# Kernel tuning notes

Measured on AMD Instinct MI355X. Metric: run time of the kernel, lower is better.

## Reference

```python
import jax, jax.numpy as jnp
import numpy as np

B, T, H, DQK, DV = 2, 8192, 8, 128, 128
HID = H * DQK  # 1024
CHUNK = 64
EPS = 1e-5


def hedgehog(x, w, b):
    # torch Linear: y = x @ W.T + b, then softmax over cat([2y, -2y])
    y = x @ w.T + b
    return jax.nn.softmax(jnp.concatenate([2.0 * y, -2.0 * y], axis=-1), axis=-1)


def rmsnorm(x):
    return x * jax.lax.rsqrt(jnp.mean(x * x, axis=-1, keepdims=True) + EPS)


def chunk_linear_attn(q, k, v):
    # q, k: [B, T, H, Dk]; v: [B, T, H, Dv]  (head_first=False)
    scale = q.shape[-1] ** -0.5
    q = q * scale
    Bq, Tq, Hq, Dk = q.shape
    Dv = v.shape[-1]
    nc = Tq // CHUNK

    def to_chunks(t):
        # [B, T, H, D] -> [nc, B, H, C, D]
        return t.reshape(Bq, nc, CHUNK, Hq, -1).transpose(1, 0, 3, 2, 4)

    qc, kc, vc = to_chunks(q), to_chunks(k), to_chunks(v)
    mask = jnp.tril(jnp.ones((CHUNK, CHUNK), dtype=bool))

    def step(S, qkv):
        qi, ki, vi = qkv  # [B, H, C, D]
        attn = jnp.einsum('bhcd,bhed->bhce', qi, ki)      # intra-chunk scores
        attn = jnp.where(mask, attn, 0.0)                 # causal within chunk
        o = jnp.einsum('bhce,bhev->bhcv', attn, vi) \
            + jnp.einsum('bhcd,bhdv->bhcv', qi, S)        # inter-chunk via state
        S = S + jnp.einsum('bhcd,bhcv->bhdv', ki, vi)
        return S, o

    S0 = jnp.zeros((Bq, Hq, Dk, Dv), q.dtype)
    _, oc = jax.lax.scan(step, S0, (qc, kc, vc))          # oc: [nc, B, H, C, Dv]
    return oc.transpose(1, 0, 3, 2, 4).reshape(Bq, Tq, Hq, Dv)


def setup_inputs() -> dict:
    key = jax.random.key(0)
    ks = jax.random.split(key, 9)
    gain = 2.0 ** (-2.5)

    def xavier(k, shape):
        bound = gain * np.sqrt(6.0 / (shape[0] + shape[1]))
        return jax.random.uniform(k, shape, jnp.float32, -bound, bound)

    return {
        'x': jax.random.normal(ks[0], (B, T, HID), jnp.float32),
        'Wq': xavier(ks[1], (HID, HID)),
        'Wk': xavier(ks[2], (HID, HID)),
        'Wv': xavier(ks[3], (HID, HID)),
        'Wo': xavier(ks[4], (HID, HID)),
        # self.apply xavier-inits the hedgehog Linear layers too (no _is_hf_initialized flag)
        'fmq_w': xavier(ks[5], (DQK, DQK)),
        'fmq_b': jnp.zeros((DQK,), jnp.float32),
        'fmk_w': xavier(ks[6], (DQK, DQK)),
        'fmk_b': jnp.zeros((DQK,), jnp.float32),
    }


def reference(x, Wq, Wk, Wv, Wo, fmq_w, fmq_b, fmk_w, fmk_b):
    q = (x @ Wq.T).reshape(B, T, H, DQK)
    k = (x @ Wk.T).reshape(B, T, H, DQK)
    v = (x @ Wv.T).reshape(B, T, H, DV)
    q = hedgehog(q, fmq_w, fmq_b)   # [B, T, H, 2*DQK]
    k = hedgehog(k, fmk_w, fmk_b)   # [B, T, H, 2*DQK]
    o = chunk_linear_attn(q, k, v)  # [B, T, H, DV]
    o = rmsnorm(o.reshape(B, T, H * DV))
    return o @ Wo.T
```

## Files before the change

kernel.cpp:

```cpp
#include <hip/hip_runtime.h>
#include <stdint.h>

typedef unsigned short u16;
typedef __bf16 bf16x8 __attribute__((ext_vector_type(8)));
typedef float f32x4 __attribute__((ext_vector_type(4)));
typedef float f32x16 __attribute__((ext_vector_type(16)));

__device__ __forceinline__ u16 f2b(float f) {
  union { float f; unsigned u; } v; v.f = f;
  unsigned r = v.u + 0x7fffu + ((v.u >> 16) & 1u);
  return (u16)(r >> 16);
}
__device__ __forceinline__ float b2f(u16 b) {
  union { unsigned u; float f; } v; v.u = ((unsigned)b) << 16;
  return v.f;
}

__global__ __launch_bounds__(256) void cast_bf16(const float* __restrict__ in,
                                                 u16* __restrict__ out, int n4) {
  int i = blockIdx.x * 256 + threadIdx.x;
  if (i >= n4) return;
  float4 f = ((const float4*)in)[i];
  ushort4 r = make_ushort4(f2b(f.x), f2b(f.y), f2b(f.z), f2b(f.w));
  ((ushort4*)out)[i] = r;
}

__global__ __launch_bounds__(256) void fold_w(const float* __restrict__ W,
                                              const float* __restrict__ fmw,
                                              u16* __restrict__ out) {
  int hj = blockIdx.x;
  int h = hj >> 7, j = hj & 127;
  int i0 = threadIdx.x * 4;
  float a0 = 0.f, a1 = 0.f, a2 = 0.f, a3 = 0.f;
  const float* Wh = W + (size_t)(h * 128) * 1024 + i0;
  const float* fw = fmw + j * 128;
  for (int d = 0; d < 128; ++d) {
    float wv = fw[d];
    const float* wr = Wh + (size_t)d * 1024;
    a0 += wv * wr[0]; a1 += wv * wr[1]; a2 += wv * wr[2]; a3 += wv * wr[3];
  }
  ushort4 r = make_ushort4(f2b(a0), f2b(a1), f2b(a2), f2b(a3));
  ((ushort4*)(out + (size_t)hj * 1024))[threadIdx.x] = r;
}

template <int OUT_BF16>
__global__ __launch_bounds__(256) void gemm_bt(const u16* __restrict__ A,
                                               const u16* __restrict__ B,
                                               void* __restrict__ Cv,
                                               int M, int N, int K, int SWZ, int LNT) {
  __shared__ u16 smem[16384];
  u16* As = smem;
  u16* Bs = smem + 8192;
  const int tid = threadIdx.x;
  int g = blockIdx.y * gridDim.x + blockIdx.x;
  int xcd = g & 7, local = g >> 3;
  int mt, nt;
  if (SWZ == 0) {
    mt = xcd * ((int)gridDim.y >> 3) + (local >> LNT);
    nt = local & ((1 << LNT) - 1);
  } else {
    nt = xcd * ((int)gridDim.x >> 3) + (local >> 3);
    mt = local & 7;
  }
  const int m0 = mt * 128, n0 = nt * 128;
  const int wave = tid >> 6, lane = tid & 63;
  const int wm = (wave >> 1) << 6, wn = (wave & 1) << 6;
  f32x4 acc[4][4] = {};
  const int srow = tid >> 3;
  const int scol = (tid & 7) << 3;
  const u16* Ab = A + (size_t)(m0 + srow) * K + scol;
  const u16* Bb = B + (size_t)(n0 + srow) * K + scol;
  u16* Asp = As + srow * 64 + scol;
  u16* Bsp = Bs + srow * 64 + scol;
  const int fm = lane & 15;
  const int fk = (lane >> 4) << 3;
  for (int kt = 0; kt < K; kt += 64) {
#pragma unroll
    for (int i = 0; i < 4; ++i) {
      __builtin_amdgcn_global_load_lds(
          (__attribute__((address_space(1))) unsigned int*)(Ab + (size_t)i * 32 * K + kt),
          (__attribute__((address_space(3))) unsigned int*)(Asp + i * 32 * 64), 16, 0, 0);
      __builtin_amdgcn_global_load_lds(
          (__attribute__((address_space(1))) unsigned int*)(Bb + (size_t)i * 32 * K + kt),
          (__attribute__((address_space(3))) unsigned int*)(Bsp + i * 32 * 64), 16, 0, 0);
    }
    __syncthreads();
#pragma unroll
    for (int kb = 0; kb < 2; ++kb) {
      bf16x8 af[4], bfr[4];
#pragma unroll
      for (int i = 0; i < 4; ++i)
        af[i] = *(const bf16x8*)(As + (wm + i * 16 + fm) * 64 + kb * 32 + fk);
#pragma unroll
      for (int j = 0; j < 4; ++j)
        bfr[j] = *(const bf16x8*)(Bs + (wn + j * 16 + fm) * 64 + kb * 32 + fk);
#pragma unroll
      for (int i = 0; i < 4; ++i)
#pragma unroll
        for (int j = 0; j < 4; ++j)
          acc[i][j] = __builtin_amdgcn_mfma_f32_16x16x32_bf16(af[i], bfr[j], acc[i][j], 0, 0, 0);
    }
    __syncthreads();
  }
  const int cr = (lane >> 4) << 2;
  const int cc = lane & 15;
  if (OUT_BF16) {
    u16* Cs = smem;
#pragma unroll
    for (int i = 0; i < 4; ++i)
#pragma unroll
      for (int j = 0; j < 4; ++j)
#pragma unroll
        for (int r = 0; r < 4; ++r)
          Cs[(wm + i * 16 + cr + r) * 128 + wn + j * 16 + cc] = f2b(acc[i][j][r]);
    __syncthreads();
    u16* Cg = (u16*)Cv;
#pragma unroll
    for (int i = 0; i < 8; ++i) {
      int row = (i >> 1) * 32 + (tid >> 3);
      int col = ((i & 1) * 8 + (tid & 7)) * 8;
      *(uint4*)(Cg + (size_t)(m0 + row) * N + n0 + col) = *(const uint4*)(Cs + row * 128 + col);
    }
  } else {
    float* Csf = (float*)smem;
    float* Cg = (float*)Cv;
#pragma unroll
    for (int hh = 0; hh < 2; ++hh) {
      __syncthreads();
      if ((wm >> 6) == hh) {
#pragma unroll
        for (int i = 0; i < 4; ++i)
#pragma unroll
          for (int j = 0; j < 4; ++j)
#pragma unroll
            for (int r = 0; r < 4; ++r)
              Csf[(i * 16 + cr + r) * 128 + wn + j * 16 + cc] = acc[i][j][r];
      }
      __syncthreads();
#pragma unroll
      for (int i = 0; i < 8; ++i) {
        int row = (i >> 1) * 16 + (tid >> 4);
        int col = ((i & 1) * 16 + (tid & 15)) * 4;
        *(float4*)(Cg + (size_t)(m0 + hh * 64 + row) * N + n0 + col) =
            *(const float4*)(Csf + row * 128 + col);
      }
    }
  }
}

__global__ __launch_bounds__(256) void hedgehog_sm(const u16* __restrict__ y,
                                                   const float* __restrict__ bias,
                                                   u16* __restrict__ phi, float scale,
                                                   int colbase) {
  int wave = threadIdx.x >> 6, lane = threadIdx.x & 63;
  int rh = blockIdx.x * 4 + wave;
  const u16* yr = y + (size_t)(rh >> 3) * 2048 + colbase + (rh & 7) * 128;
  float a1 = 2.f * (b2f(yr[lane]) + bias[lane]);
  float a2 = 2.f * (b2f(yr[lane + 64]) + bias[lane + 64]);
  float mx = fmaxf(fabsf(a1), fabsf(a2));
#pragma unroll
  for (int off = 32; off; off >>= 1) mx = fmaxf(mx, __shfl_xor(mx, off, 64));
  float e1 = __expf(a1 - mx), e2 = __expf(a2 - mx);
  float n1 = __expf(-a1 - mx), n2 = __expf(-a2 - mx);
  float s = e1 + e2 + n1 + n2;
#pragma unroll
  for (int off = 32; off; off >>= 1) s += __shfl_xor(s, off, 64);
  float inv = scale / s;
  u16* pr = phi + (size_t)rh * 256;
  pr[lane] = f2b(e1 * inv);
  pr[lane + 64] = f2b(e2 * inv);
  pr[lane + 128] = f2b(n1 * inv);
  pr[lane + 192] = f2b(n2 * inv);
}

__global__ __launch_bounds__(256, 1) void attn_intra_kv2(const u16* __restrict__ phi_q,
                                                         const u16* __restrict__ phi_k,
                                                         const u16* __restrict__ vt,
                                                         float* __restrict__ o,
                                                         u16* __restrict__ kv) {
  __shared__ u16 lds[18432];
  u16* At = lds;
  u16* Kt = lds;
  int g = blockIdx.x;
  int n = g & 63, h = g >> 6;
  int t0 = n * 128;
  const u16* qg = phi_q + ((size_t)t0 * 8 + h) * 256;
  const u16* kg = phi_k + ((size_t)t0 * 8 + h) * 256;
  const u16* vg = vt + (size_t)(h * 128) * 8192 + t0;
  int tid = threadIdx.x, lane = tid & 63, w = tid >> 6;
  const int fr = lane & 31, fg = (lane >> 5) << 3;
  const int rbase = (lane >> 5) << 2;
  const int mw = (w >> 1) << 6;
  const int nw = (w & 1) << 6;

  f32x16 accS[2][2] = {};
#pragma unroll
  for (int ks = 0; ks < 16; ++ks) {
    bf16x8 a[2], b[2];
#pragma unroll
    for (int i = 0; i < 2; ++i)
      a[i] = *(const bf16x8*)(qg + (size_t)(mw + i * 32 + fr) * 2048 + ks * 16 + fg);
#pragma unroll
    for (int j = 0; j < 2; ++j)
      b[j] = *(const bf16x8*)(kg + (size_t)(nw + j * 32 + fr) * 2048 + ks * 16 + fg);
#pragma unroll
    for (int i = 0; i < 2; ++i)
#pragma unroll
      for (int j = 0; j < 2; ++j)
        accS[i][j] = __builtin_amdgcn_mfma_f32_32x32x16_bf16(a[i], b[j], accS[i][j], 0, 0, 0);
  }
#pragma unroll
  for (int i = 0; i < 2; ++i)
#pragma unroll
    for (int j = 0; j < 2; ++j) {
      int col = nw + j * 32 + (lane & 31);
#pragma unroll
      for (int r = 0; r < 16; ++r) {
        int row = mw + i * 32 + (r & 3) + ((r >> 2) << 3) + rbase;
        At[row * 136 + col] = f2b(col <= row ? accS[i][j][r] : 0.f);
      }
    }
  __syncthreads();
  f32x16 accO[2][2] = {};
#pragma unroll
  for (int ks = 0; ks < 8; ++ks) {
    bf16x8 a[2], b[2];
#pragma unroll
    for (int i = 0; i < 2; ++i)
      a[i] = *(const bf16x8*)(At + (mw + i * 32 + fr) * 136 + ks * 16 + fg);
#pragma unroll
    for (int j = 0; j < 2; ++j)
      b[j] = *(const bf16x8*)(vg + (size_t)(nw + j * 32 + fr) * 8192 + ks * 16 + fg);
#pragma unroll
    for (int i = 0; i < 2; ++i)
#pragma unroll
      for (int j = 0; j < 2; ++j)
        accO[i][j] = __builtin_amdgcn_mfma_f32_32x32x16_bf16(a[i], b[j], accO[i][j], 0, 0, 0);
  }
  {
    float* og = o + ((size_t)t0 * 8 + h) * 128;
#pragma unroll
    for (int i = 0; i < 2; ++i)
#pragma unroll
      for (int j = 0; j < 2; ++j) {
        int vc = nw + j * 32 + (lane & 31);
#pragma unroll
        for (int r = 0; r < 16; ++r) {
          int row = mw + i * 32 + (r & 3) + ((r >> 2) << 3) + rbase;
          og[(size_t)row * 1024 + vc] = accO[i][j][r];
        }
      }
  }
  __syncthreads();

  const int nd = w << 6;
  f32x16 accKV[4][2] = {};
#pragma unroll
  for (int hb = 0; hb < 2; ++hb) {
    {
      int r4 = (tid & 15) << 2;
      int d0 = (tid >> 4) << 4;
      u16 tmp[4][16];
#pragma unroll
      for (int r = 0; r < 4; ++r) {
        const u16* src = kg + (size_t)(hb * 64 + r4 + r) * 2048 + d0;
        *(uint4*)(tmp[r]) = *(const uint4*)src;
        *(uint4*)(tmp[r] + 8) = *(const uint4*)(src + 8);
      }
#pragma unroll
      for (int jj = 0; jj < 16; ++jj) {
        ushort4 pk = make_ushort4(tmp[0][jj], tmp[1][jj], tmp[2][jj], tmp[3][jj]);
        *(ushort4*)(Kt + (d0 + jj) * 72 + r4) = pk;
      }
    }
    __syncthreads();
#pragma unroll
    for (int ks = 0; ks < 4; ++ks) {
      bf16x8 a[4], b[2];
#pragma unroll
      for (int mi = 0; mi < 4; ++mi)
        a[mi] = *(const bf16x8*)(vg + (size_t)(mi * 32 + fr) * 8192 + hb * 64 + ks * 16 + fg);
#pragma unroll
      for (int nj = 0; nj < 2; ++nj)
        b[nj] = *(const bf16x8*)(Kt + (nd + nj * 32 + fr) * 72 + ks * 16 + fg);
#pragma unroll
      for (int mi = 0; mi < 4; ++mi)
#pragma unroll
        for (int nj = 0; nj < 2; ++nj)
          accKV[mi][nj] =
              __builtin_amdgcn_mfma_f32_32x32x16_bf16(a[mi], b[nj], accKV[mi][nj], 0, 0, 0);
    }
    __syncthreads();
  }
  {
    u16* kvg = kv + (size_t)g * 32768;
#pragma unroll
    for (int mi = 0; mi < 4; ++mi)
#pragma unroll
      for (int nj = 0; nj < 2; ++nj) {
        f32x16 acc = accKV[mi][nj];
        int d = nd + nj * 32 + (lane & 31);
#pragma unroll
        for (int r = 0; r < 16; ++r) {
          int vc = mi * 32 + (r & 3) + ((r >> 2) << 3) + rbase;
          kvg[(size_t)vc * 256 + d] = f2b(acc[r]);
        }
      }
  }
}

__global__ __launch_bounds__(256) void kv_scan2(u16* __restrict__ kv) {
  int idx = blockIdx.x * 256 + threadIdx.x;
  int h = idx >> 13;
  int e4 = idx & 8191;
  u16* p = kv + (size_t)h * 2097152 + (size_t)e4 * 4;
  float run[4] = {};
  for (int nn = 0; nn < 64; ++nn) {
    uint2 raw = *(const uint2*)p;
    u16* rv = (u16*)&raw;
    uint2 outw;
    u16* ov = (u16*)&outw;
#pragma unroll
    for (int i = 0; i < 4; ++i) {
      float v = b2f(rv[i]);
      ov[i] = f2b(run[i]);
      run[i] += v;
    }
    *(uint2*)p = outw;
    p += 32768;
  }
}

__global__ __launch_bounds__(256, 1) void attn_inter2(const u16* __restrict__ phi_q,
                                                      const u16* __restrict__ kv,
                                                      float* __restrict__ o) {
  int g = blockIdx.x;
  int n = g & 63, h = g >> 6;
  int t0 = n * 128;
  const u16* qg = phi_q + ((size_t)t0 * 8 + h) * 256;
  const u16* sg = kv + (size_t)g * 32768;
  int tid = threadIdx.x, lane = tid & 63, w = tid >> 6;
  const int fr = lane & 31, fg = (lane >> 5) << 3;
  const int rbase = (lane >> 5) << 2;
  const int mw = (w >> 1) << 6;
  const int nw = (w & 1) << 6;
  f32x16 acc[2][2] = {};
#pragma unroll
  for (int ks = 0; ks < 16; ++ks) {
    bf16x8 a[2], b[2];
#pragma unroll
    for (int i = 0; i < 2; ++i)
      a[i] = *(const bf16x8*)(qg + (size_t)(mw + i * 32 + fr) * 2048 + ks * 16 + fg);
#pragma unroll
    for (int j = 0; j < 2; ++j)
      b[j] = *(const bf16x8*)(sg + (size_t)(nw + j * 32 + fr) * 256 + ks * 16 + fg);
#pragma unroll
    for (int i = 0; i < 2; ++i)
#pragma unroll
      for (int j = 0; j < 2; ++j)
        acc[i][j] = __builtin_amdgcn_mfma_f32_32x32x16_bf16(a[i], b[j], acc[i][j], 0, 0, 0);
  }
  float* og = o + ((size_t)t0 * 8 + h) * 128;
#pragma unroll
  for (int i = 0; i < 2; ++i)
#pragma unroll
    for (int j = 0; j < 2; ++j) {
      int vc = nw + j * 32 + (lane & 31);
#pragma unroll
      for (int r = 0; r < 16; ++r) {
        int row = mw + i * 32 + (r & 3) + ((r >> 2) << 3) + rbase;
        og[(size_t)row * 1024 + vc] += acc[i][j][r];
      }
    }
}

__global__ __launch_bounds__(256) void rmsnorm_k(const float* __restrict__ o,
                                                 u16* __restrict__ on) {
  __shared__ float red[4];
  int row = blockIdx.x;
  const float* orow = o + (size_t)row * 1024;
  int tid = threadIdx.x;
  float4 v = ((const float4*)orow)[tid];
  float ss = v.x * v.x + v.y * v.y + v.z * v.z + v.w * v.w;
#pragma unroll
  for (int off = 32; off; off >>= 1) ss += __shfl_xor(ss, off, 64);
  if ((tid & 63) == 0) red[tid >> 6] = ss;
  __syncthreads();
  float tot = red[0] + red[1] + red[2] + red[3];
  float rms = rsqrtf(tot * (1.f / 1024.f) + 1e-5f);
  ushort4 r = make_ushort4(f2b(v.x * rms), f2b(v.y * rms), f2b(v.z * rms), f2b(v.w * rms));
  ((ushort4*)(on + (size_t)row * 1024))[tid] = r;
}

extern "C" void kernel_launch(void* const* d_in, const int* in_sizes, int n_in,
                              void* d_out, int out_size, void* d_ws, size_t ws_size,
                              hipStream_t stream) {
  const float* x     = (const float*)d_in[0];
  const float* Wq    = (const float*)d_in[1];
  const float* Wk    = (const float*)d_in[2];
  const float* Wv    = (const float*)d_in[3];
  const float* Wo    = (const float*)d_in[4];
  const float* fmq_w = (const float*)d_in[5];
  const float* fmq_b = (const float*)d_in[6];
  const float* fmk_w = (const float*)d_in[7];
  const float* fmk_b = (const float*)d_in[8];

  char* ws = (char*)d_ws;
  u16*   kvb  = (u16*)(ws + 0);
  u16*   xb   = (u16*)(ws + 0);
  u16*   yb   = (u16*)(ws + 16777216);
  u16*   onb  = (u16*)(ws + 50331648);
  u16*   phiq = (u16*)(ws + 67108864);
  u16*   phik = (u16*)(ws + 100663296);
  u16*   vtb  = (u16*)(ws + 134217728);
  float* obuf = (float*)(ws + 150994944);
  u16*   wqkc = (u16*)(ws + 184549376);
  u16*   wvb  = (u16*)(ws + 188743680);
  u16*   wob  = (u16*)(ws + 190840832);

  cast_bf16<<<1024, 256, 0, stream>>>(Wv, wvb, 262144);
  cast_bf16<<<1024, 256, 0, stream>>>(Wo, wob, 262144);
  fold_w<<<1024, 256, 0, stream>>>(Wq, fmq_w, wqkc);
  fold_w<<<1024, 256, 0, stream>>>(Wk, fmk_w, wqkc + 1048576);

  for (int b = 0; b < 2; ++b) {
    const float* xsrc = x + (size_t)b * 8388608;
    float* osrc = (float*)d_out + (size_t)b * 8388608;
    cast_bf16<<<8192, 256, 0, stream>>>(xsrc, xb, 2097152);
    gemm_bt<1><<<dim3(16, 64), 256, 0, stream>>>(xb, wqkc, yb, 8192, 2048, 1024, 0, 4);
    hedgehog_sm<<<16384, 256, 0, stream>>>(yb, fmq_b, phiq, 0.0625f, 0);
    hedgehog_sm<<<16384, 256, 0, stream>>>(yb, fmk_b, phik, 1.0f, 1024);
    gemm_bt<1><<<dim3(64, 8), 256, 0, stream>>>(wvb, xb, vtb, 1024, 8192, 1024, 1, 0);
    attn_intra_kv2<<<512, 256, 0, stream>>>(phiq, phik, vtb, obuf, kvb);
    kv_scan2<<<256, 256, 0, stream>>>(kvb);
    attn_inter2<<<512, 256, 0, stream>>>(phiq, kvb, obuf);
    rmsnorm_k<<<8192, 256, 0, stream>>>(obuf, onb);
    gemm_bt<0><<<dim3(8, 64), 256, 0, stream>>>(onb, wob, osrc, 8192, 1024, 1024, 0, 3);
  }
}
```

Before: 696.7 us.

## Add 256x256-tile pipelined bf16 GEMM for fused Q/K projection

Adds a new 512-thread GEMM kernel with 256x256 output tiles, swizzled LDS layout, and direct global-to-LDS async loads. It is multi-stage double-buffered with setprio around the MFMA bursts. It replaces the generic gemm_bt for the x·[Wq;Wk]-folded projection, aiming to raise data reuse per tile and overlap loads with MFMA compute. The larger LDS footprint (128KB) limits occupancy and relies on the dimensions dividing evenly by 256.

```diff
diff --git a/kernel.cpp b/kernel.cpp
--- a/kernel.cpp
+++ b/kernel.cpp
@@ -14,6 +14,10 @@
 __device__ __forceinline__ float b2f(u16 b) {
   union { unsigned u; float f; } v; v.u = ((unsigned)b) << 16;
   return v.f;
+}
+
+__device__ __forceinline__ int swz64(int b) {
+  return b ^ (((((b >> 6) & 3) ^ ((b >> 8) & 1))) << 4);
 }
 
 __global__ __launch_bounds__(256) void cast_bf16(const float* __restrict__ in,
@@ -41,6 +45,159 @@
   }
   ushort4 r = make_ushort4(f2b(a0), f2b(a1), f2b(a2), f2b(a3));
   ((ushort4*)(out + (size_t)hj * 1024))[threadIdx.x] = r;
+}
+
+__global__ __launch_bounds__(512, 2) void gemm256(const u16* __restrict__ A,
+                                                  const u16* __restrict__ B,
+                                                  u16* __restrict__ C,
+                                                  int M, int N, int K, int LNT) {
+  __shared__ u16 lds[65536];
+  const int tid = threadIdx.x, w = tid >> 6, lane = tid & 63;
+  int g = blockIdx.x;
+  int wg = (g & 7) * ((int)gridDim.x >> 3) + (g >> 3);
+  const int nt = wg & ((1 << LNT) - 1), mt = wg >> LNT;
+  const int m0 = mt << 8, n0 = nt << 8;
+  const int wm = w >> 2, wn = w & 3;
+  const int fm = lane & 15, fkb = (lane >> 4) << 4;
+
+  int so0 = w * 1024 + lane * 16;
+  int so1 = so0 + 8192;
+  const int p0s = swz64(so0), p1s = swz64(so1);
+  const size_t ga0 = (size_t)(p0s >> 6) * K + ((p0s & 63) >> 1);
+  const size_t ga1 = (size_t)(p1s >> 6) * K + ((p1s & 63) >> 1);
+  so0 >>= 1; so1 >>= 1;
+#define STAGE(g0, slot)                                                               \
+  do {                                                                                \
+    __builtin_amdgcn_global_load_lds(                                                 \
+        (const __attribute__((address_space(1))) unsigned int*)((g0) + ga0),          \
+        (__attribute__((address_space(3))) unsigned int*)((slot) + so0), 16, 0, 0);   \
+    __builtin_amdgcn_global_load_lds(                                                 \
+        (const __attribute__((address_space(1))) unsigned int*)((g0) + ga1),          \
+        (__attribute__((address_space(3))) unsigned int*)((slot) + so1), 16, 0, 0);   \
+  } while (0)
+
+  int aoff[2][4], boff[4];
+#pragma unroll
+  for (int mh = 0; mh < 2; ++mh)
+#pragma unroll
+    for (int mi = 0; mi < 4; ++mi)
+      aoff[mh][mi] = swz64((wm * 128 + mh * 64 + mi * 16 + fm) * 64 + fkb) >> 1;
+#pragma unroll
+  for (int ni = 0; ni < 4; ++ni)
+    boff[ni] = swz64((wn * 64 + ni * 16 + fm) * 64 + fkb) >> 1;
+
+  const u16* Ag = A + (size_t)m0 * K;
+  const u16* Bg = B + (size_t)n0 * K;
+  const int NT = K >> 6;
+  f32x4 acc[8][4] = {};
+
+  STAGE(Ag, lds);
+  STAGE(Bg, lds + 32768);
+  STAGE(Ag + 32, lds + 8192);
+  STAGE(Bg + 32, lds + 32768 + 8192);
+  STAGE(Ag + 64, lds + 16384);
+  STAGE(Bg + 64, lds + 32768 + 16384);
+  asm volatile("s_waitcnt vmcnt(4)" ::: "memory");
+  __builtin_amdgcn_s_barrier();
+
+  for (int t = 0; t < NT; ++t) {
+    const int buf = t & 1, nb = buf ^ 1;
+    const u16* As0 = lds + buf * 16384;
+    const u16* As1 = As0 + 8192;
+    const u16* Bs0 = lds + 32768 + buf * 16384;
+    const u16* Bs1 = Bs0 + 8192;
+    bf16x8 a[4], bfr[4];
+
+#pragma unroll
+    for (int mi = 0; mi < 4; ++mi) a[mi] = *(const bf16x8*)(As0 + aoff[0][mi]);
+#pragma unroll
+    for (int ni = 0; ni < 4; ++ni) bfr[ni] = *(const bf16x8*)(Bs0 + boff[ni]);
+    if (t + 1 < NT) STAGE(Ag + (t + 1) * 64 + 32, lds + nb * 16384 + 8192);
+    __builtin_amdgcn_s_barrier();
+    asm volatile("s_waitcnt lgkmcnt(0)" ::: "memory");
+    __builtin_amdgcn_sched_barrier(0);
+    __builtin_amdgcn_s_setprio(1);
+#pragma unroll
+    for (int mi = 0; mi < 4; ++mi)
+#pragma unroll
+      for (int ni = 0; ni < 4; ++ni)
+        acc[mi][ni] = __builtin_amdgcn_mfma_f32_16x16x32_bf16(a[mi], bfr[ni], acc[mi][ni], 0, 0, 0);
+    __builtin_amdgcn_s_setprio(0);
+    __builtin_amdgcn_s_barrier();
+
+#pragma unroll
+    for (int mi = 0; mi < 4; ++mi) a[mi] = *(const bf16x8*)(As0 + aoff[1][mi]);
+    if (t + 1 < NT) STAGE(Bg + (t + 1) * 64 + 32, lds + 32768 + nb * 16384 + 8192);
+    __builtin_amdgcn_s_barrier();
+    asm volatile("s_waitcnt lgkmcnt(0)" ::: "memory");
+    __builtin_amdgcn_sched_barrier(0);
+    __builtin_amdgcn_s_setprio(1);
+#pragma unroll
+    for (int mi = 0; mi < 4; ++mi)
+#pragma unroll
+      for (int ni = 0; ni < 4; ++ni)
+        acc[4 + mi][ni] =
+            __builtin_amdgcn_mfma_f32_16x16x32_bf16(a[mi], bfr[ni], acc[4 + mi][ni], 0, 0, 0);
+    __builtin_amdgcn_s_setprio(0);
+    __builtin_amdgcn_s_barrier();
+
+#pragma unroll
+    for (int mi = 0; mi < 4; ++mi) a[mi] = *(const bf16x8*)(As1 + aoff[0][mi]);
+#pragma unroll
+    for (int ni = 0; ni < 4; ++ni) bfr[ni] = *(const bf16x8*)(Bs1 + boff[ni]);
+    if (t + 2 < NT) STAGE(Ag + (t + 2) * 64, lds + buf * 16384);
+    __builtin_amdgcn_s_barrier();
+    asm volatile("s_waitcnt lgkmcnt(0)" ::: "memory");
+    __builtin_amdgcn_sched_barrier(0);
+    __builtin_amdgcn_s_setprio(1);
+#pragma unroll
+    for (int mi = 0; mi < 4; ++mi)
+#pragma unroll
+      for (int ni = 0; ni < 4; ++ni)
+        acc[mi][ni] = __builtin_amdgcn_mfma_f32_16x16x32_bf16(a[mi], bfr[ni], acc[mi][ni], 0, 0, 0);
+    __builtin_amdgcn_s_setprio(0);
+    __builtin_amdgcn_s_barrier();
+
+#pragma unroll
+    for (int mi = 0; mi < 4; ++mi) a[mi] = *(const bf16x8*)(As1 + aoff[1][mi]);
+    if (t + 2 < NT) STAGE(Bg + (t + 2) * 64, lds + 32768 + buf * 16384);
+    __builtin_amdgcn_s_barrier();
+    asm volatile("s_waitcnt lgkmcnt(0)" ::: "memory");
+    __builtin_amdgcn_sched_barrier(0);
+    __builtin_amdgcn_s_setprio(1);
+#pragma unroll
+    for (int mi = 0; mi < 4; ++mi)
+#pragma unroll
+      for (int ni = 0; ni < 4; ++ni)
+        acc[4 + mi][ni] =
+            __builtin_amdgcn_mfma_f32_16x16x32_bf16(a[mi], bfr[ni], acc[4 + mi][ni], 0, 0, 0);
+    __builtin_amdgcn_s_setprio(0);
+    if (t < NT - 2)
+      asm volatile("s_waitcnt vmcnt(4)" ::: "memory");
+    else
+      asm volatile("s_waitcnt vmcnt(0)" ::: "memory");
+    __builtin_amdgcn_s_barrier();
+  }
+#undef STAGE
+
+  u16* Cs = lds;
+  const int cr = (lane >> 4) << 2, cc = lane & 15;
+#pragma unroll
+  for (int am = 0; am < 8; ++am)
+#pragma unroll
+    for (int ni = 0; ni < 4; ++ni)
+#pragma unroll
+      for (int r = 0; r < 4; ++r)
+        Cs[(wm * 128 + (am >> 2) * 64 + (am & 3) * 16 + cr + r) * 256 + wn * 64 + ni * 16 + cc] =
+            f2b(acc[am][ni][r]);
+  __syncthreads();
+#pragma unroll
+  for (int pass = 0; pass < 16; ++pass) {
+    int row = pass * 16 + (tid >> 5);
+    int colb = (tid & 31) << 4;
+    *(uint4*)((char*)(C + (size_t)(m0 + row) * N + n0) + colb) =
+        *(const uint4*)((const char*)(Cs + row * 256) + colb);
+  }
 }
 
 template <int OUT_BF16>
@@ -427,7 +584,7 @@
     const float* xsrc = x + (size_t)b * 8388608;
     float* osrc = (float*)d_out + (size_t)b * 8388608;
     cast_bf16<<<8192, 256, 0, stream>>>(xsrc, xb, 2097152);
-    gemm_bt<1><<<dim3(16, 64), 256, 0, stream>>>(xb, wqkc, yb, 8192, 2048, 1024, 0, 4);
+    gemm256<<<256, 512, 0, stream>>>(xb, wqkc, yb, 8192, 2048, 1024, 3);
     hedgehog_sm<<<16384, 256, 0, stream>>>(yb, fmq_b, phiq, 0.0625f, 0);
     hedgehog_sm<<<16384, 256, 0, stream>>>(yb, fmk_b, phik, 1.0f, 1024);
     gemm_bt<1><<<dim3(64, 8), 256, 0, stream>>>(wvb, xb, vtb, 1024, 8192, 1024, 1, 0);
```

Result: faster. 666.2 us (-4.4%).
